# Performance work log

Measured on AMD Instinct MI355X. Metric: run time of the kernel, lower is better.

The kernel has to match this reference:

```python
import jax, jax.numpy as jnp
import numpy as np

# Graph geometry: G complete graphs (molecules) of n nodes each.
N_PER_G, G, DEG = 64, 256, 16
H, D = 8, 8
IN_DIM = H * D      # 64
EDGE_DIM = 64
N = N_PER_G * G                      # 16384 nodes
EF = G * N_PER_G * N_PER_G           # 1,048,576 full edges
ES = G * N_PER_G * DEG               # 262,144 sparse edges
SCALE = float(np.sqrt(D))


def _edges():
    n = N_PER_G
    # full graph: all (i -> j) pairs per block, edge id = b*n*n + i*n + j
    ij = np.arange(n * n)
    i, j = ij // n, ij % n
    b = np.arange(G)[:, None]
    src_full = (b * n + i[None, :]).reshape(-1).astype(np.int32)
    dst_full = (b * n + j[None, :]).reshape(-1).astype(np.int32)
    # sparse graph: each dst j receives from DEG distinct sources (j+1..j+DEG mod n)
    jj = np.arange(n)[:, None]
    kk = np.arange(DEG)[None, :]
    ii = (jj + 1 + kk) % n
    eid_block = (ii * n + jj).reshape(-1)                 # [n*DEG]
    sparse_eid = (np.arange(G)[:, None] * n * n + eid_block[None, :]).reshape(-1).astype(np.int32)
    return jnp.asarray(src_full), jnp.asarray(dst_full), jnp.asarray(sparse_eid)


def setup_inputs() -> dict:
    key = jax.random.key(0)
    ks = jax.random.split(key, 16)
    w = lambda k, shape, s=0.05: s * jax.random.normal(k, shape, jnp.float32)
    src_full, dst_full, sparse_eid = _edges()
    return dict(
        h=jax.random.normal(ks[0], (N, IN_DIM), jnp.float32),
        e=jax.random.normal(ks[1], (ES, EDGE_DIM), jnp.float32),
        adj2=jax.random.uniform(ks[2], (EF,), jnp.float32),
        rel_pos_3d=jax.random.normal(ks[3], (EF, H), jnp.float32),
        Wq=w(ks[4], (H * D, IN_DIM)), bq=jnp.zeros((H * D,), jnp.float32),
        Wk=w(ks[5], (H * D, IN_DIM)), bk=jnp.zeros((H * D,), jnp.float32),
        Wv=w(ks[6], (H * D, IN_DIM)), bv=jnp.zeros((H * D,), jnp.float32),
        Wpe=w(ks[7], (H, EDGE_DIM)), bpe=jnp.zeros((H,), jnp.float32),
        Wap=w(ks[8], (EDGE_DIM, H)), bap=jnp.zeros((EDGE_DIM,), jnp.float32),
        Wo=w(ks[9], (H * D, H * D)), bo=jnp.zeros((H * D,), jnp.float32),
        Woe=w(ks[10], (EDGE_DIM, EDGE_DIM)), boe=jnp.zeros((EDGE_DIM,), jnp.float32),
        src_full=src_full, dst_full=dst_full, sparse_eid=sparse_eid,
    )


def reference(h, e, adj2, rel_pos_3d, Wq, bq, Wk, bk, Wv, bv, Wpe, bpe,
              Wap, bap, Wo, bo, Woe, boe, src_full, dst_full, sparse_eid):
    Qh = (h @ Wq.T + bq).reshape(N, H, D)
    Kh = (h @ Wk.T + bk).reshape(N, H, D)
    Vh = (h @ Wv.T + bv).reshape(N, H, D)
    proj_e = e @ Wpe.T + bpe                                   # [ES, H]
    # edge-wise QK dot (src=K, dst=Q), scaled, then gaussian-decay + rel-pos bias
    score = jnp.sum(Kh[src_full] * Qh[dst_full], axis=-1) / SCALE   # [EF, H]
    score = score * adj2[:, None] + rel_pos_3d                      # [EF, H]
    # gather sparse-subgraph scores, project for edge output, add proj_e bias
    sc_sp = score[sparse_eid]                                        # [ES, H]
    e_out_raw = sc_sp @ Wap.T + bap                                  # [ES, EDGE_DIM]
    score = score.at[sparse_eid].set(sc_sp + proj_e)
    # edge softmax over incoming edges of each destination node
    logits = jnp.clip(score, -5.0, 5.0)
    m = jax.ops.segment_max(logits, dst_full, num_segments=N)
    ex = jnp.exp(logits - m[dst_full])
    den = jax.ops.segment_sum(ex, dst_full, num_segments=N)
    attn = ex / den[dst_full]                                        # [EF, H]
    # weighted scatter-sum of source values
    wV = jax.ops.segment_sum(Vh[src_full] * attn[..., None], dst_full, num_segments=N)
    h_out = wV.reshape(N, H * D) @ Wo.T + bo
    e_out = (e_out_raw + e) @ Woe.T + boe
    return h_out, e_out
```

## Files before the change

### kernel.cpp

```cpp
#include <hip/hip_runtime.h>


__global__ __launch_bounds__(512, 2) void qkv_kernel(
    const float* __restrict__ h,
    const float* __restrict__ Wq, const float* __restrict__ bq,
    const float* __restrict__ Wk, const float* __restrict__ bk,
    const float* __restrict__ Wv, const float* __restrict__ bv,
    float* __restrict__ Qs, float* __restrict__ Ks, float* __restrict__ Vs)
{
    const int b    = blockIdx.x;
    const int t    = threadIdx.x;
    const int lane = t & 63;
    const int wu   = __builtin_amdgcn_readfirstlane(t >> 6);

    const float* hrow = h + (size_t)(b * 64 + lane) * 64;
    float accQ[8], accK[8], accV[8];
    #pragma unroll
    for (int cc = 0; cc < 8; ++cc) {
        const int c = wu * 8 + cc;
        accQ[cc] = bq[c]; accK[cc] = bk[c]; accV[cc] = bv[c];
    }
    #pragma unroll 1
    for (int k0 = 0; k0 < 4; ++k0) {
        float hv[16];
        #pragma unroll
        for (int u = 0; u < 4; ++u) {
            const float4 x = ((const float4*)hrow)[k0 * 4 + u];
            hv[u*4+0] = x.x; hv[u*4+1] = x.y; hv[u*4+2] = x.z; hv[u*4+3] = x.w;
        }
        #pragma unroll
        for (int cc = 0; cc < 8; ++cc) {
            const int c = wu * 8 + cc;
            const float* wq  = Wq + c * 64 + k0 * 16;
            const float* wk  = Wk + c * 64 + k0 * 16;
            const float* wvp = Wv + c * 64 + k0 * 16;
            #pragma unroll
            for (int k = 0; k < 16; ++k) {
                accQ[cc] = fmaf(hv[k], wq[k],  accQ[cc]);
                accK[cc] = fmaf(hv[k], wk[k],  accK[cc]);
                accV[cc] = fmaf(hv[k], wvp[k], accV[cc]);
            }
        }
    }
    const size_t o = (size_t)(b * 64 + lane) * 64 + wu * 8;
    *(float4*)(Qs + o)     = make_float4(accQ[0], accQ[1], accQ[2], accQ[3]);
    *(float4*)(Qs + o + 4) = make_float4(accQ[4], accQ[5], accQ[6], accQ[7]);
    *(float4*)(Ks + o)     = make_float4(accK[0], accK[1], accK[2], accK[3]);
    *(float4*)(Ks + o + 4) = make_float4(accK[4], accK[5], accK[6], accK[7]);
    *(float4*)(Vs + o)     = make_float4(accV[0], accV[1], accV[2], accV[3]);
    *(float4*)(Vs + o + 4) = make_float4(accV[4], accV[5], accV[6], accV[7]);
}

__global__ __launch_bounds__(256, 2) void pe_kernel(
    const float* __restrict__ e,
    const float* __restrict__ Wpe, const float* __restrict__ bpe,
    float* __restrict__ PEs)
{
    const int row = blockIdx.x * 256 + threadIdx.x;
    const float* erow = e + (size_t)row * 64;
    float acc[8];
    #pragma unroll
    for (int h2 = 0; h2 < 8; ++h2) acc[h2] = bpe[h2];
    #pragma unroll 1
    for (int k0 = 0; k0 < 4; ++k0) {
        float ev[16];
        #pragma unroll
        for (int u = 0; u < 4; ++u) {
            const float4 x = ((const float4*)erow)[k0 * 4 + u];
            ev[u*4+0] = x.x; ev[u*4+1] = x.y; ev[u*4+2] = x.z; ev[u*4+3] = x.w;
        }
        #pragma unroll
        for (int h2 = 0; h2 < 8; ++h2) {
            const float* wp = Wpe + h2 * 64 + k0 * 16;
            #pragma unroll
            for (int k = 0; k < 16; ++k)
                acc[h2] = fmaf(ev[k], wp[k], acc[h2]);
        }
    }
    float* p0 = PEs + (size_t)row * 8;
    *(float4*)(p0)     = make_float4(acc[0], acc[1], acc[2], acc[3]);
    *(float4*)(p0 + 4) = make_float4(acc[4], acc[5], acc[6], acc[7]);
}

__global__ __launch_bounds__(512, 2) void attn_kernel(
    const float* __restrict__ Qs, const float* __restrict__ Ks,
    const float* __restrict__ Vs, const float* __restrict__ PEs,
    const float* __restrict__ adj2,
    const float* __restrict__ rel,
    const float* __restrict__ Wo, const float* __restrict__ bo,
    float* __restrict__ h_out,
    float* __restrict__ scsp)
{
    __shared__ float shK[64 * 64];
    __shared__ float shV[64 * 64];
    __shared__ float shPE[512 * 8];
    __shared__ float shSC[512 * 8];

    const int b2   = blockIdx.x;
    const int b    = b2 >> 1;
    const int joff = (b2 & 1) << 5;
    const int t    = threadIdx.x;

    {
        const int r = t >> 3, g = t & 7;
        const int d = r * 64 + ((g ^ (r & 7)) << 3);
        const float* kp = Ks + (size_t)b * 4096 + t * 8;
        const float* vp = Vs + (size_t)b * 4096 + t * 8;
        *(float4*)&shK[d]     = *(const float4*)(kp);
        *(float4*)&shK[d + 4] = *(const float4*)(kp + 4);
        *(float4*)&shV[d]     = *(const float4*)(vp);
        *(float4*)&shV[d + 4] = *(const float4*)(vp + 4);
        const float* pp = PEs + ((size_t)b * 1024 + joff * 16 + t) * 8;
        *(float4*)&shPE[t * 8]     = *(const float4*)(pp);
        *(float4*)&shPE[t * 8 + 4] = *(const float4*)(pp + 4);
    }
    const int j_local = t >> 4;
    const int hh      = (t >> 1) & 7;
    const int half    = t & 1;
    const int j       = joff + j_local;
    float q[8];
    {
        const float* qp = Qs + (size_t)(b * 64 + j) * 64 + hh * 8;
        const float4 a = *(const float4*)qp;
        const float4 c = *(const float4*)(qp + 4);
        q[0]=a.x; q[1]=a.y; q[2]=a.z; q[3]=a.w;
        q[4]=c.x; q[5]=c.y; q[6]=c.z; q[7]=c.w;
    }
    __syncthreads();

    float den = 0.f;
    float wv[8] = {0.f,0.f,0.f,0.f,0.f,0.f,0.f,0.f};
    const float* adjB = adj2 + (size_t)b * 4096 + j;
    const float* relB = rel  + ((size_t)b * 4096 + j) * 8 + hh;
    const float inv_scale = 0.35355339059327379f;
    #pragma unroll 4
    for (int it = 0; it < 32; ++it) {
        const int i  = (half << 5) + it;
        const float a2 = adjB[(size_t)i * 64];
        const float rp = relB[(size_t)i * 512];
        const int kb = i * 64 + ((hh ^ (i & 7)) << 3);
        const float4 kA = *(const float4*)&shK[kb];
        const float4 kB = *(const float4*)&shK[kb + 4];
        float s;
        s = kA.x * q[0];
        s = fmaf(kA.y, q[1], s); s = fmaf(kA.z, q[2], s); s = fmaf(kA.w, q[3], s);
        s = fmaf(kB.x, q[4], s); s = fmaf(kB.y, q[5], s); s = fmaf(kB.z, q[6], s);
        s = fmaf(kB.w, q[7], s);
        s = fmaf(s * inv_scale, a2, rp);
        const int kidx = (i - j - 1) & 63;
        if (kidx < 16) {
            const int sl = j_local * 16 + kidx;
            shSC[sl * 8 + hh] = s;
            s += shPE[sl * 8 + hh];
        }
        s = fminf(fmaxf(s, -5.f), 5.f);
        const float ex = __expf(s);
        den += ex;
        const float4 vA = *(const float4*)&shV[kb];
        const float4 vB = *(const float4*)&shV[kb + 4];
        wv[0] = fmaf(ex, vA.x, wv[0]); wv[1] = fmaf(ex, vA.y, wv[1]);
        wv[2] = fmaf(ex, vA.z, wv[2]); wv[3] = fmaf(ex, vA.w, wv[3]);
        wv[4] = fmaf(ex, vB.x, wv[4]); wv[5] = fmaf(ex, vB.y, wv[5]);
        wv[6] = fmaf(ex, vB.z, wv[6]); wv[7] = fmaf(ex, vB.w, wv[7]);
    }
    den += __shfl_xor(den, 1);
    #pragma unroll
    for (int u = 0; u < 8; ++u) wv[u] += __shfl_xor(wv[u], 1);
    __syncthreads();
    if (half == 0) {
        const float id = 1.f / den;
        float* wp = &shPE[j_local * 64 + hh * 8];
        *(float4*)(wp)     = make_float4(wv[0]*id, wv[1]*id, wv[2]*id, wv[3]*id);
        *(float4*)(wp + 4) = make_float4(wv[4]*id, wv[5]*id, wv[6]*id, wv[7]*id);
    }
    {
        const float4 a = *(const float4*)&shSC[t * 8];
        const float4 c = *(const float4*)&shSC[t * 8 + 4];
        float* sp = scsp + (size_t)((size_t)b * 1024 + joff * 16 + t) * 8;
        *(float4*)(sp)     = a;
        *(float4*)(sp + 4) = c;
    }
    __syncthreads();

    {
        const int rl = t >> 4;
        const int cq = t & 15;
        float acc[4];
        #pragma unroll
        for (int u = 0; u < 4; ++u) acc[u] = bo[cq * 4 + u];
        #pragma unroll
        for (int k0 = 0; k0 < 4; ++k0) {
            float tv[16];
            #pragma unroll
            for (int u = 0; u < 4; ++u) {
                const float4 x = *(const float4*)&shPE[rl * 64 + k0 * 16 + u * 4];
                tv[u*4+0] = x.x; tv[u*4+1] = x.y; tv[u*4+2] = x.z; tv[u*4+3] = x.w;
            }
            #pragma unroll
            for (int u = 0; u < 4; ++u) {
                const float* wo = Wo + (cq * 4 + u) * 64 + k0 * 16;
                #pragma unroll
                for (int k = 0; k < 16; ++k)
                    acc[u] = fmaf(tv[k], wo[k], acc[u]);
            }
        }
        float* orow = h_out + (size_t)(b * 64 + joff + rl) * 64 + cq * 4;
        *(float4*)orow = make_float4(acc[0], acc[1], acc[2], acc[3]);
    }
}

__global__ void prep_kernel(const float* __restrict__ Wap, const float* __restrict__ bap,
                            const float* __restrict__ Woe, const float* __restrict__ boe,
                            float* __restrict__ M2)
{
    const int t = blockIdx.x * 64 + threadIdx.x;
    if (t < 512) {
        const int c = t >> 3, hq = t & 7;
        float s = 0.f;
        #pragma unroll 8
        for (int k = 0; k < 64; ++k) s = fmaf(Woe[c * 64 + k], Wap[k * 8 + hq], s);
        M2[t] = s;
    } else if (t < 576) {
        const int c = t - 512;
        float s = boe[c];
        #pragma unroll 8
        for (int k = 0; k < 64; ++k) s = fmaf(bap[k], Woe[c * 64 + k], s);
        M2[512 + c] = s;
    }
}

template<int M2G>
__global__ __launch_bounds__(256, 2) void eout_kernel(
    const float* __restrict__ e,
    const float* __restrict__ scsp,
    const float* __restrict__ Wap, const float* __restrict__ bap,
    const float* __restrict__ Woe, const float* __restrict__ boe,
    const float* __restrict__ M2g,
    float* __restrict__ e_out, int sstride)
{
    __shared__ float shE[64 * 64];
    __shared__ float shS[64 * 8];
    __shared__ float shM[576];

    const int t    = threadIdx.x;
    const int base = blockIdx.x * 64;

    {
        const int r = t >> 2, qq = t & 3;
        const float* ep = e + (size_t)(base + r) * 64 + qq * 16;
        #pragma unroll
        for (int u = 0; u < 4; ++u) {
            const float4 x = ((const float4*)ep)[u];
            const int cc = qq * 4 + u;
            *(float4*)&shE[r * 64 + ((cc ^ (r & 15)) << 2)] = x;
        }
    }
    if (t < 128) {
        const int r = t >> 1, pp = t & 1;
        *(float4*)&shS[r * 8 + pp * 4] =
            *(const float4*)(scsp + (size_t)(base + r) * sstride + pp * 4);
    }
    if (!M2G) {
        #pragma unroll
        for (int z = 0; z < 2; ++z) {
            const int idx = t * 2 + z;
            const int c = idx >> 3, hq = idx & 7;
            float s = 0.f;
            for (int k = 0; k < 64; ++k) s = fmaf(Woe[c * 64 + k], Wap[k * 8 + hq], s);
            shM[idx] = s;
        }
        if (t < 64) {
            float s = boe[t];
            for (int k = 0; k < 64; ++k) s = fmaf(bap[k], Woe[t * 64 + k], s);
            shM[512 + t] = s;
        }
    }
    __syncthreads();

    const int w = __builtin_amdgcn_readfirstlane(t >> 6);
    const int r = t & 63;

    float sc[8];
    {
        const float4 a  = *(const float4*)&shS[r * 8];
        const float4 c4 = *(const float4*)&shS[r * 8 + 4];
        sc[0]=a.x; sc[1]=a.y; sc[2]=a.z; sc[3]=a.w;
        sc[4]=c4.x; sc[5]=c4.y; sc[6]=c4.z; sc[7]=c4.w;
    }
    float acc[16];
    #pragma unroll
    for (int u = 0; u < 16; ++u) {
        const int c = w * 16 + u;
        float s = M2G ? M2g[512 + c] : shM[512 + c];
        #pragma unroll
        for (int hq = 0; hq < 8; ++hq)
            s = fmaf(sc[hq], (M2G ? M2g[c * 8 + hq] : shM[c * 8 + hq]), s);
        acc[u] = s;
    }
    #pragma unroll
    for (int k0 = 0; k0 < 4; ++k0) {
        float ev[16];
        #pragma unroll
        for (int v = 0; v < 4; ++v) {
            const int cc = k0 * 4 + v;
            const float4 x = *(const float4*)&shE[r * 64 + ((cc ^ (r & 15)) << 2)];
            ev[v*4+0] = x.x; ev[v*4+1] = x.y; ev[v*4+2] = x.z; ev[v*4+3] = x.w;
        }
        #pragma unroll
        for (int u = 0; u < 16; ++u) {
            const float* wr = Woe + (w * 16 + u) * 64 + k0 * 16;
            #pragma unroll
            for (int k = 0; k < 16; ++k)
                acc[u] = fmaf(ev[k], wr[k], acc[u]);
        }
    }
    float* orow = e_out + (size_t)(base + r) * 64 + w * 16;
    #pragma unroll
    for (int u = 0; u < 4; ++u)
        *(float4*)&orow[u * 4] =
            make_float4(acc[u*4+0], acc[u*4+1], acc[u*4+2], acc[u*4+3]);
}

extern "C" void kernel_launch(void* const* d_in, const int* in_sizes, int n_in,
                              void* d_out, int out_size, void* d_ws, size_t ws_size,
                              hipStream_t stream) {
    const float* h    = (const float*)d_in[0];
    const float* e    = (const float*)d_in[1];
    const float* adj2 = (const float*)d_in[2];
    const float* rel  = (const float*)d_in[3];
    const float* Wq   = (const float*)d_in[4];  const float* bq  = (const float*)d_in[5];
    const float* Wk   = (const float*)d_in[6];  const float* bk  = (const float*)d_in[7];
    const float* Wv   = (const float*)d_in[8];  const float* bv  = (const float*)d_in[9];
    const float* Wpe  = (const float*)d_in[10]; const float* bpe = (const float*)d_in[11];
    const float* Wap  = (const float*)d_in[12]; const float* bap = (const float*)d_in[13];
    const float* Wo   = (const float*)d_in[14]; const float* bo  = (const float*)d_in[15];
    const float* Woe  = (const float*)d_in[16]; const float* boe = (const float*)d_in[17];

    float* out  = (float*)d_out;
    float* hout = out;
    float* eout = out + 16384 * 64;
    float* Qs   = eout;
    float* Ks   = eout + 1048576;
    float* Vs   = eout + 2097152;
    float* PEs  = eout + 3145728;
    float* ws   = (float*)d_ws;
    float* scsp = ws;
    float* M2g  = ws + 2097152;

    prep_kernel<<<dim3(9), dim3(64), 0, stream>>>(Wap, bap, Woe, boe, M2g);
    qkv_kernel<<<dim3(256), dim3(512), 0, stream>>>(
        h, Wq, bq, Wk, bk, Wv, bv, Qs, Ks, Vs);
    pe_kernel<<<dim3(1024), dim3(256), 0, stream>>>(e, Wpe, bpe, PEs);
    attn_kernel<<<dim3(512), dim3(512), 0, stream>>>(
        Qs, Ks, Vs, PEs, adj2, rel, Wo, bo, hout, scsp);
    eout_kernel<1><<<dim3(4096), dim3(256), 0, stream>>>(
        e, scsp, Wap, bap, Woe, boe, M2g, eout, 8);
}
```

Measured before the change: 161.5 us.

## Merge QKV and edge-PE projection kernels; reuse shared buffers in attention

The Q/K/V projection and the edge proj_e projection now run as one launch: the first 256 blocks compute QKV and the remaining 512 blocks compute PE rows. This removes one kernel launch and lets the two independent projections run concurrently on the GPU. In the attention kernel the separate score scratch buffer is dropped by writing raw sparse scores back into the PE slot after reading it. The normalized wV tile is staged in the K shared buffer instead, which cuts LDS use to raise occupancy. The Wo loop is also no longer unrolled.

After: 142.2 us. 1.14x faster.

```diff
diff --git a/kernel.cpp b/kernel.cpp
--- a/kernel.cpp
+++ b/kernel.cpp
@@ -1,85 +1,83 @@
 #include <hip/hip_runtime.h>
 
 
-__global__ __launch_bounds__(512, 2) void qkv_kernel(
+__global__ __launch_bounds__(512, 2) void qkvpe_kernel(
     const float* __restrict__ h,
+    const float* __restrict__ e,
     const float* __restrict__ Wq, const float* __restrict__ bq,
     const float* __restrict__ Wk, const float* __restrict__ bk,
     const float* __restrict__ Wv, const float* __restrict__ bv,
-    float* __restrict__ Qs, float* __restrict__ Ks, float* __restrict__ Vs)
+    const float* __restrict__ Wpe, const float* __restrict__ bpe,
+    float* __restrict__ Qs, float* __restrict__ Ks, float* __restrict__ Vs,
+    float* __restrict__ PEs)
 {
-    const int b    = blockIdx.x;
-    const int t    = threadIdx.x;
-    const int lane = t & 63;
-    const int wu   = __builtin_amdgcn_readfirstlane(t >> 6);
-
-    const float* hrow = h + (size_t)(b * 64 + lane) * 64;
-    float accQ[8], accK[8], accV[8];
-    #pragma unroll
-    for (int cc = 0; cc < 8; ++cc) {
-        const int c = wu * 8 + cc;
-        accQ[cc] = bq[c]; accK[cc] = bk[c]; accV[cc] = bv[c];
-    }
-    #pragma unroll 1
-    for (int k0 = 0; k0 < 4; ++k0) {
-        float hv[16];
-        #pragma unroll
-        for (int u = 0; u < 4; ++u) {
-            const float4 x = ((const float4*)hrow)[k0 * 4 + u];
-            hv[u*4+0] = x.x; hv[u*4+1] = x.y; hv[u*4+2] = x.z; hv[u*4+3] = x.w;
-        }
+    const int t = threadIdx.x;
+    if (blockIdx.x < 256) {
+        const int b    = blockIdx.x;
+        const int lane = t & 63;
+        const int wu   = __builtin_amdgcn_readfirstlane(t >> 6);
+        const float* hrow = h + (size_t)(b * 64 + lane) * 64;
+        float accQ[8], accK[8], accV[8];
         #pragma unroll
         for (int cc = 0; cc < 8; ++cc) {
             const int c = wu * 8 + cc;
-            const float* wq  = Wq + c * 64 + k0 * 16;
-            const float* wk  = Wk + c * 64 + k0 * 16;
-            const float* wvp = Wv + c * 64 + k0 * 16;
-            #pragma unroll
-            for (int k = 0; k < 16; ++k) {
-                accQ[cc] = fmaf(hv[k], wq[k],  accQ[cc]);
-                accK[cc] = fmaf(hv[k], wk[k],  accK[cc]);
-                accV[cc] = fmaf(hv[k], wvp[k], accV[cc]);
-            }
-        }
-    }
-    const size_t o = (size_t)(b * 64 + lane) * 64 + wu * 8;
-    *(float4*)(Qs + o)     = make_float4(accQ[0], accQ[1], accQ[2], accQ[3]);
-    *(float4*)(Qs + o + 4) = make_float4(accQ[4], accQ[5], accQ[6], accQ[7]);
-    *(float4*)(Ks + o)     = make_float4(accK[0], accK[1], accK[2], accK[3]);
-    *(float4*)(Ks + o + 4) = make_float4(accK[4], accK[5], accK[6], accK[7]);
-    *(float4*)(Vs + o)     = make_float4(accV[0], accV[1], accV[2], accV[3]);
-    *(float4*)(Vs + o + 4) = make_float4(accV[4], accV[5], accV[6], accV[7]);
-}
-
-__global__ __launch_bounds__(256, 2) void pe_kernel(
-    const float* __restrict__ e,
-    const float* __restrict__ Wpe, const float* __restrict__ bpe,
-    float* __restrict__ PEs)
-{
-    const int row = blockIdx.x * 256 + threadIdx.x;
-    const float* erow = e + (size_t)row * 64;
-    float acc[8];
-    #pragma unroll
-    for (int h2 = 0; h2 < 8; ++h2) acc[h2] = bpe[h2];
-    #pragma unroll 1
-    for (int k0 = 0; k0 < 4; ++k0) {
-        float ev[16];
-        #pragma unroll
-        for (int u = 0; u < 4; ++u) {
-            const float4 x = ((const float4*)erow)[k0 * 4 + u];
-            ev[u*4+0] = x.x; ev[u*4+1] = x.y; ev[u*4+2] = x.z; ev[u*4+3] = x.w;
-        }
-        #pragma unroll
-        for (int h2 = 0; h2 < 8; ++h2) {
-            const float* wp = Wpe + h2 * 64 + k0 * 16;
-            #pragma unroll
-            for (int k = 0; k < 16; ++k)
-                acc[h2] = fmaf(ev[k], wp[k], acc[h2]);
-        }
-    }
-    float* p0 = PEs + (size_t)row * 8;
-    *(float4*)(p0)     = make_float4(acc[0], acc[1], acc[2], acc[3]);
-    *(float4*)(p0 + 4) = make_float4(acc[4], acc[5], acc[6], acc[7]);
+            accQ[cc] = bq[c]; accK[cc] = bk[c]; accV[cc] = bv[c];
+        }
+        #pragma unroll 1
+        for (int k0 = 0; k0 < 4; ++k0) {
+            float hv[16];
+            #pragma unroll
+            for (int u = 0; u < 4; ++u) {
+                const float4 x = ((const float4*)hrow)[k0 * 4 + u];
+                hv[u*4+0] = x.x; hv[u*4+1] = x.y; hv[u*4+2] = x.z; hv[u*4+3] = x.w;
+            }
+            #pragma unroll
+            for (int cc = 0; cc < 8; ++cc) {
+                const int c = wu * 8 + cc;
+                const float* wq  = Wq + c * 64 + k0 * 16;
+                const float* wk  = Wk + c * 64 + k0 * 16;
+                const float* wvp = Wv + c * 64 + k0 * 16;
+                #pragma unroll
+                for (int k = 0; k < 16; ++k) {
+                    accQ[cc] = fmaf(hv[k], wq[k],  accQ[cc]);
+                    accK[cc] = fmaf(hv[k], wk[k],  accK[cc]);
+                    accV[cc] = fmaf(hv[k], wvp[k], accV[cc]);
+                }
+            }
+        }
+        const size_t o = (size_t)(b * 64 + lane) * 64 + wu * 8;
+        *(float4*)(Qs + o)     = make_float4(accQ[0], accQ[1], accQ[2], accQ[3]);
+        *(float4*)(Qs + o + 4) = make_float4(accQ[4], accQ[5], accQ[6], accQ[7]);
+        *(float4*)(Ks + o)     = make_float4(accK[0], accK[1], accK[2], accK[3]);
+        *(float4*)(Ks + o + 4) = make_float4(accK[4], accK[5], accK[6], accK[7]);
+        *(float4*)(Vs + o)     = make_float4(accV[0], accV[1], accV[2], accV[3]);
+        *(float4*)(Vs + o + 4) = make_float4(accV[4], accV[5], accV[6], accV[7]);
+    } else {
+        const int row = (blockIdx.x - 256) * 512 + t;
+        const float* erow = e + (size_t)row * 64;
+        float acc[8];
+        #pragma unroll
+        for (int h2 = 0; h2 < 8; ++h2) acc[h2] = bpe[h2];
+        #pragma unroll 1
+        for (int k0 = 0; k0 < 4; ++k0) {
+            float ev[16];
+            #pragma unroll
+            for (int u = 0; u < 4; ++u) {
+                const float4 x = ((const float4*)erow)[k0 * 4 + u];
+                ev[u*4+0] = x.x; ev[u*4+1] = x.y; ev[u*4+2] = x.z; ev[u*4+3] = x.w;
+            }
+            #pragma unroll
+            for (int h2 = 0; h2 < 8; ++h2) {
+                const float* wp = Wpe + h2 * 64 + k0 * 16;
+                #pragma unroll
+                for (int k = 0; k < 16; ++k)
+                    acc[h2] = fmaf(ev[k], wp[k], acc[h2]);
+            }
+        }
+        float* p0 = PEs + (size_t)row * 8;
+        *(float4*)(p0)     = make_float4(acc[0], acc[1], acc[2], acc[3]);
+        *(float4*)(p0 + 4) = make_float4(acc[4], acc[5], acc[6], acc[7]);
+    }
 }
 
 __global__ __launch_bounds__(512, 2) void attn_kernel(
@@ -94,7 +92,6 @@
     __shared__ float shK[64 * 64];
     __shared__ float shV[64 * 64];
     __shared__ float shPE[512 * 8];
-    __shared__ float shSC[512 * 8];
 
     const int b2   = blockIdx.x;
     const int b    = b2 >> 1;
@@ -149,9 +146,10 @@
         s = fmaf(s * inv_scale, a2, rp);
         const int kidx = (i - j - 1) & 63;
         if (kidx < 16) {
-            const int sl = j_local * 16 + kidx;
-            shSC[sl * 8 + hh] = s;
-            s += shPE[sl * 8 + hh];
+            const int x = (j_local * 16 + kidx) * 8 + hh;
+            const float pe = shPE[x];
+            shPE[x] = s;
+            s += pe;
         }
         s = fminf(fmaxf(s, -5.f), 5.f);
         const float ex = __expf(s);
@@ -167,19 +165,20 @@
     #pragma unroll
     for (int u = 0; u < 8; ++u) wv[u] += __shfl_xor(wv[u], 1);
     __syncthreads();
-    if (half == 0) {
-        const float id = 1.f / den;
-        float* wp = &shPE[j_local * 64 + hh * 8];
-        *(float4*)(wp)     = make_float4(wv[0]*id, wv[1]*id, wv[2]*id, wv[3]*id);
-        *(float4*)(wp + 4) = make_float4(wv[4]*id, wv[5]*id, wv[6]*id, wv[7]*id);
-    }
-    {
-        const float4 a = *(const float4*)&shSC[t * 8];
-        const float4 c = *(const float4*)&shSC[t * 8 + 4];
+
+    {
+        const float4 a = *(const float4*)&shPE[t * 8];
+        const float4 c = *(const float4*)&shPE[t * 8 + 4];
         float* sp = scsp + (size_t)((size_t)b * 1024 + joff * 16 + t) * 8;
         *(float4*)(sp)     = a;
         *(float4*)(sp + 4) = c;
     }
+    if (half == 0) {
+        const float id = 1.f / den;
+        float* wp = &shK[j_local * 64 + hh * 8];
+        *(float4*)(wp)     = make_float4(wv[0]*id, wv[1]*id, wv[2]*id, wv[3]*id);
+        *(float4*)(wp + 4) = make_float4(wv[4]*id, wv[5]*id, wv[6]*id, wv[7]*id);
+    }
     __syncthreads();
 
     {
@@ -188,12 +187,12 @@
         float acc[4];
         #pragma unroll
         for (int u = 0; u < 4; ++u) acc[u] = bo[cq * 4 + u];
-        #pragma unroll
+        #pragma unroll 1
         for (int k0 = 0; k0 < 4; ++k0) {
             float tv[16];
             #pragma unroll
             for (int u = 0; u < 4; ++u) {
-                const float4 x = *(const float4*)&shPE[rl * 64 + k0 * 16 + u * 4];
+                const float4 x = *(const float4*)&shK[rl * 64 + k0 * 16 + u * 4];
                 tv[u*4+0] = x.x; tv[u*4+1] = x.y; tv[u*4+2] = x.z; tv[u*4+3] = x.w;
             }
             #pragma unroll
@@ -348,9 +347,8 @@
     float* M2g  = ws + 2097152;
 
     prep_kernel<<<dim3(9), dim3(64), 0, stream>>>(Wap, bap, Woe, boe, M2g);
-    qkv_kernel<<<dim3(256), dim3(512), 0, stream>>>(
-        h, Wq, bq, Wk, bk, Wv, bv, Qs, Ks, Vs);
-    pe_kernel<<<dim3(1024), dim3(256), 0, stream>>>(e, Wpe, bpe, PEs);
+    qkvpe_kernel<<<dim3(768), dim3(512), 0, stream>>>(
+        h, e, Wq, bq, Wk, bk, Wv, bv, Wpe, bpe, Qs, Ks, Vs, PEs);
     attn_kernel<<<dim3(512), dim3(512), 0, stream>>>(
         Qs, Ks, Vs, PEs, adj2, rel, Wo, bo, hout, scsp);
     eout_kernel<1><<<dim3(4096), dim3(256), 0, stream>>>(
```
